# Kernel optimization log

Hardware: AMD Instinct MI355X
Metric: run time of the kernel (lower is better)

Reference implementation:

```python
import jax, jax.numpy as jnp
import numpy as np
from jax import lax

L, B, H, Z, V = 64, 32, 256, 256, 32000  # steps, max_ast_depth, hidden=units, latent, vocab


def setup_inputs() -> dict:
    key = jax.random.key(0)
    ks = jax.random.split(key, 32)
    p = lambda i, shape: jax.random.normal(ks[i], shape, dtype=jnp.float32) * 0.05
    inp = {
        "nodes": jax.random.randint(ks[0], (L, B), 0, V),
        "edges": jax.random.randint(ks[1], (L, B), 0, 2) > 0,
        "enc_init": jax.random.normal(ks[2], (B, H), dtype=jnp.float32) * 0.001,
        "eps": jax.random.normal(ks[3], (B, Z), dtype=jnp.float32),
        "emb": p(4, (V, H)),
    }
    for j, n in enumerate(["enc_c", "enc_s", "dec_c", "dec_s"]):
        inp[n + "_Wih"] = p(5 + 4 * j, (3 * H, H))
        inp[n + "_Whh"] = p(6 + 4 * j, (3 * H, H))
        inp[n + "_bih"] = p(7 + 4 * j, (3 * H,))
        inp[n + "_bhh"] = p(8 + 4 * j, (3 * H,))
    inp["W_mean"] = p(21, (Z, H)); inp["b_mean"] = p(22, (Z,))
    inp["W_logv"] = p(23, (Z, H)); inp["b_logv"] = p(24, (Z,))
    inp["W_l2h"] = p(25, (H, Z)); inp["b_l2h"] = p(26, (H,))
    inp["W_voc"] = p(27, (V, H)); inp["b_voc"] = p(28, (V,))
    return inp


def _gru_cell(Wih, Whh, bih, bhh, x, h):
    # torch.nn.GRU single-layer cell; x, h: [B, H]
    gi = x @ Wih.T + bih
    gh = h @ Whh.T + bhh
    ir, iz, inn = jnp.split(gi, 3, axis=-1)
    hr, hz, hn = jnp.split(gh, 3, axis=-1)
    r = jax.nn.sigmoid(ir + hr)
    zg = jax.nn.sigmoid(iz + hz)
    n = jnp.tanh(inn + r * hn)
    return (1.0 - zg) * n + zg * h


def _tree_rnn(pc, ps, emb_nodes, edges, h0):
    # emb_nodes: [L, B, H], edges: [L, B] bool, h0: [B, H]
    # each step runs child & sibling GRUs on the SAME state, selects per node by edge
    def step(h, xe):
        x, e = xe
        hc = _gru_cell(*pc, x, h)
        hs = _gru_cell(*ps, x, h)
        h_new = jnp.where(e[:, None], hc, hs)
        return h_new, h_new  # 1-layer GRU, seq_len 1: output == new state
    h_final, outs = lax.scan(step, h0, (emb_nodes, edges))
    return outs, h_final  # outs: [L, B, H]


def reference(nodes, edges, enc_init, eps, emb,
              enc_c_Wih, enc_c_Whh, enc_c_bih, enc_c_bhh,
              enc_s_Wih, enc_s_Whh, enc_s_bih, enc_s_bhh,
              dec_c_Wih, dec_c_Whh, dec_c_bih, dec_c_bhh,
              dec_s_Wih, dec_s_Whh, dec_s_bih, dec_s_bhh,
              W_mean, b_mean, W_logv, b_logv, W_l2h, b_l2h, W_voc, b_voc):
    x = emb[nodes]  # [L, B, H]
    _, h_enc = _tree_rnn((enc_c_Wih, enc_c_Whh, enc_c_bih, enc_c_bhh),
                         (enc_s_Wih, enc_s_Whh, enc_s_bih, enc_s_bhh),
                         x, edges, enc_init)
    mean = h_enc @ W_mean.T + b_mean          # [B, Z]
    logv = h_enc @ W_logv.T + b_logv
    z = eps * jnp.exp(0.5 * logv) + mean      # reparameterization
    h0 = z @ W_l2h.T + b_l2h                  # decoder initial state [B, H]
    outs, _ = _tree_rnn((dec_c_Wih, dec_c_Whh, dec_c_bih, dec_c_bhh),
                        (dec_s_Wih, dec_s_Whh, dec_s_bih, dec_s_bhh),
                        x, edges, h0)         # [L, B, H]
    logits = outs @ W_voc.T + b_voc           # [L, B, V]
    logp = jax.nn.log_softmax(logits, axis=-1)
    return logp, mean, logv, z
```

## Files before the change

### kernel.cpp

```cpp
#include <hip/hip_runtime.h>
#include <stdint.h>

typedef unsigned short u16;
typedef unsigned int u32;

#define L_STEPS 64
#define B_SZ 32
#define H_SZ 256
#define Z_SZ 256
#define V_SZ 32000
#define H2 128
#define G3H 768

typedef _Float16 h2_t __attribute__((ext_vector_type(2)));
typedef _Float16 f16x8 __attribute__((ext_vector_type(8)));
typedef float f32x4 __attribute__((ext_vector_type(4)));

#define WHH2_OFF   0
#define WIH2_OFF   393216
#define WM2_OFF    786432
#define WLV2_OFF   819200
#define WL2H2_OFF  851968
#define GI2_OFF    884736
#define OUTS2_OFF  4030464
#define W16_OFF    4292608
#define WS_NEEDED  ((size_t)(W16_OFF + 4096000) * 4)

#define NPART 250

#define OUT_MEAN_OFF  65536000
#define OUT_LOGV_OFF  65544192
#define OUT_Z_OFF     65552384

__device__ __forceinline__ float fdot2(h2_t a, h2_t b, float c){
#if __has_builtin(__builtin_amdgcn_fdot2)
  return __builtin_amdgcn_fdot2(a, b, c, false);
#else
  return c + (float)a.x*(float)b.x + (float)a.y*(float)b.y;
#endif
}
__device__ __forceinline__ float sigm(float x){ return 1.f/(1.f + __expf(-x)); }

struct PackTArgs { const float2* src[11]; int n_h2[11]; int dstoff[11]; };

__global__ __launch_bounds__(256) void k_packt(PackTArgs p, h2_t* wsh){
  int m = blockIdx.y;
  int r = blockIdx.x*256 + threadIdx.x;
  if (r >= p.n_h2[m]) return;
  int row = r >> 7, k2 = r & 127;
  float2 f = p.src[m][r];
  h2_t h; h.x = (_Float16)f.x; h.y = (_Float16)f.y;
  int off = (((row>>6)*32 + (k2>>2))*64 + (row&63))*4 + (k2&3);
  wsh[p.dstoff[m] + off] = h;
}

__global__ __launch_bounds__(256) void k_packv(const float2* __restrict__ src,
                                               h2_t* __restrict__ dst, int total){
  int idx = blockIdx.x*256 + threadIdx.x;
  if (idx >= total) return;
  float2 f = src[idx];
  h2_t h; h.x = (_Float16)f.x; h.y = (_Float16)f.y;
  dst[idx] = h;
}

struct GiArgs { const float* bih[4]; };

__global__ __launch_bounds__(256) void k_gi(const int* __restrict__ nodes,
                                            const float* __restrict__ emb,
                                            const h2_t* __restrict__ wih2,
                                            GiArgs ga, h2_t* __restrict__ gi2){
  int l = blockIdx.x, g = blockIdx.y, t = threadIdx.x;
  __shared__ __align__(16) h2_t x2[B_SZ*132];
  #pragma unroll
  for (int it=0; it<16; ++it){
    int lin = it*256 + t;
    int bb = lin >> 7, k2 = lin & 127;
    int node = nodes[l*B_SZ + bb];
    float2 f = ((const float2*)(emb + (size_t)node*H_SZ))[k2];
    h2_t r; r.x=(_Float16)f.x; r.y=(_Float16)f.y;
    x2[bb*132 + k2] = r;
  }
  __syncthreads();
  const float* bih = ga.bih[g];
  for (int jc=0; jc<3; ++jc){
    int j = jc*256 + t;
    float acc[32];
    #pragma unroll
    for (int bb=0;bb<32;bb++) acc[bb]=0.f;
    const float4* Wv = (const float4*)wih2 + (size_t)g*24576 + (j>>6)*2048 + (j&63);
    #pragma unroll 2
    for (int kb=0;kb<32;kb++){
      union{float4 f; h2_t h[4];} w4;
      w4.f = Wv[kb*64];
      #pragma unroll
      for (int kc=0;kc<4;kc++){
        h2_t w = w4.h[kc];
        int k2 = kb*4 + kc;
        #pragma unroll
        for (int bb=0;bb<32;bb++) acc[bb] = fdot2(x2[bb*132+k2], w, acc[bb]);
      }
    }
    float bvv = bih[j];
    int base = (g*2048 + l*B_SZ)*384 + (j>>1);
    #pragma unroll
    for (int bb=0;bb<32;bb++){
      float own = acc[bb] + bvv;
      float oth = __shfl_xor(own, 1, 64);
      if (!(t&1)){
        h2_t r; r.x=(_Float16)own; r.y=(_Float16)oth;
        gi2[base + bb*384] = r;
      }
    }
  }
}

struct ScanArgs {
  const float* bhh[4];
  const float* b_mean; const float* b_logv; const float* b_l2h;
  const float* enc_init; const float* eps;
};

__global__ __launch_bounds__(768) void k_scan(const int* __restrict__ edges, ScanArgs sa,
                                              const h2_t* __restrict__ wsh,
                                              h2_t* __restrict__ outs2,
                                              float* __restrict__ out){
  int b = blockIdx.x, t = threadIdx.x;
  int i = t & 255, gate = t >> 8;
  int lane = t & 63, rb = t >> 6;
  __shared__ float h_lds[H_SZ];
  __shared__ __align__(16) h2_t hs2[H2];
  __shared__ float g_lds[512];
  __shared__ float s_bhh[4*G3H];
  __shared__ int s_edge[L_STEPS];
  const _Float16* gi_all = (const _Float16*)(wsh + GI2_OFF);

  if (t < H_SZ) h_lds[t] = sa.enc_init[b*H_SZ + t];
  if (t < L_STEPS) s_edge[t] = edges[t*B_SZ + b];
  #pragma unroll
  for (int m=0;m<4;m++) s_bhh[m*G3H + t] = sa.bhh[m][t];
  __syncthreads();
  if (t < H2){ h2_t r; r.x=(_Float16)h_lds[2*t]; r.y=(_Float16)h_lds[2*t+1]; hs2[t]=r; }
  __syncthreads();

  const float4* hsv = (const float4*)hs2;

  for (int ph=0; ph<2; ++ph){
    for (int l=0; l<L_STEPS; ++l){
      int e = s_edge[l];
      int gsel = (ph ? 2 : 0) + (e ? 0 : 1);
      float gi0=0.f, gi1=0.f, gi2v=0.f;
      if (t < H_SZ){
        const _Float16* gr = gi_all + (size_t)(gsel*2048 + l*B_SZ + b)*G3H;
        gi0  = (float)gr[i];
        gi1  = (float)gr[256+i];
        gi2v = (float)gr[512+i];
      }
      float bv = s_bhh[gsel*G3H + t];
      const float4* Wv = (const float4*)wsh + (size_t)gsel*24576 + rb*2048 + lane;
      float a0=0.f,a1=0.f,a2=0.f,a3=0.f;
      #pragma unroll 8
      for (int kb=0;kb<32;kb++){
        union{float4 f; h2_t h[4];} w, x;
        w.f = Wv[kb*64];
        x.f = hsv[kb];
        a0 = fdot2(x.h[0], w.h[0], a0);
        a1 = fdot2(x.h[1], w.h[1], a1);
        a2 = fdot2(x.h[2], w.h[2], a2);
        a3 = fdot2(x.h[3], w.h[3], a3);
      }
      float acc = (a0+a1)+(a2+a3) + bv;
      if (gate) g_lds[(gate-1)*256 + i] = acc;
      __syncthreads();
      if (t < H_SZ){
        float r = sigm(gi0 + acc);
        float z = sigm(gi1 + g_lds[i]);
        float n = tanhf(gi2v + r*g_lds[256+i]);
        float hn = (1.f - z)*n + z*h_lds[i];
        h_lds[i] = hn;
        float ho = __shfl_xor(hn, 1, 64);
        if (!(i & 1)){
          h2_t pk; pk.x=(_Float16)hn; pk.y=(_Float16)ho;
          hs2[i>>1] = pk;
          if (ph) outs2[(l*B_SZ + b)*H2 + (i>>1)] = pk;
        }
      }
      __syncthreads();
    }

    if (ph == 0){
      if (t < H_SZ){
        const float4* WmV = (const float4*)(wsh + WM2_OFF)  + (t>>6)*2048 + (t&63);
        const float4* WlV = (const float4*)(wsh + WLV2_OFF) + (t>>6)*2048 + (t&63);
        float m0=0.f,m1=0.f,m2=0.f,m3=0.f, l0=0.f,l1=0.f,l2=0.f,l3=0.f;
        #pragma unroll 8
        for (int kb=0;kb<32;kb++){
          union{float4 f; h2_t h[4];} wm, wl, x;
          x.f  = hsv[kb];
          wm.f = WmV[kb*64];
          wl.f = WlV[kb*64];
          m0=fdot2(x.h[0],wm.h[0],m0); m1=fdot2(x.h[1],wm.h[1],m1);
          m2=fdot2(x.h[2],wm.h[2],m2); m3=fdot2(x.h[3],wm.h[3],m3);
          l0=fdot2(x.h[0],wl.h[0],l0); l1=fdot2(x.h[1],wl.h[1],l1);
          l2=fdot2(x.h[2],wl.h[2],l2); l3=fdot2(x.h[3],wl.h[3],l3);
        }
        float am = (m0+m1)+(m2+m3) + sa.b_mean[t];
        float al = (l0+l1)+(l2+l3) + sa.b_logv[t];
        float zv = sa.eps[b*Z_SZ + t] * __expf(0.5f*al) + am;
        out[OUT_MEAN_OFF + b*Z_SZ + t] = am;
        out[OUT_LOGV_OFF + b*Z_SZ + t] = al;
        out[OUT_Z_OFF    + b*Z_SZ + t] = zv;
        h_lds[t] = zv;
      }
      __syncthreads();
      if (t < H2){ h2_t r; r.x=(_Float16)h_lds[2*t]; r.y=(_Float16)h_lds[2*t+1]; hs2[t]=r; }
      __syncthreads();
      float h0v = 0.f;
      if (t < H_SZ){
        const float4* WzV = (const float4*)(wsh + WL2H2_OFF) + (t>>6)*2048 + (t&63);
        float z0=0.f,z1=0.f,z2=0.f,z3=0.f;
        #pragma unroll 8
        for (int kb=0;kb<32;kb++){
          union{float4 f; h2_t h[4];} w, x;
          x.f = hsv[kb];
          w.f = WzV[kb*64];
          z0=fdot2(x.h[0],w.h[0],z0); z1=fdot2(x.h[1],w.h[1],z1);
          z2=fdot2(x.h[2],w.h[2],z2); z3=fdot2(x.h[3],w.h[3],z3);
        }
        h0v = (z0+z1)+(z2+z3) + sa.b_l2h[t];
      }
      __syncthreads();
      if (t < H_SZ) h_lds[t] = h0v;
      __syncthreads();
      if (t < H2){ h2_t r; r.x=(_Float16)h_lds[2*t]; r.y=(_Float16)h_lds[2*t+1]; hs2[t]=r; }
      __syncthreads();
    }
  }
}

__global__ __launch_bounds__(256) void k_gemmS(const h2_t* __restrict__ outs2,
                                               const _Float16* __restrict__ wv16,
                                               const float* __restrict__ bvoc,
                                               float* __restrict__ outf,
                                               float* __restrict__ part){
  int t = threadIdx.x;
  int lane = t & 63, w = t >> 6;
  int wm = w & 1, wn = w >> 1;
  int Mb = blockIdx.x * 64, Nb = blockIdx.y * 128;
  int lr = lane & 15, lq = lane >> 4;

  __shared__ __align__(16) _Float16 As[64*64];
  __shared__ __align__(16) _Float16 Bs[128*64];
  __shared__ float red[2][64][2];

  f32x4 acc[2][4];
  #pragma unroll
  for (int mi=0;mi<2;mi++)
    #pragma unroll
    for (int nj=0;nj<4;nj++) acc[mi][nj] = (f32x4){0.f,0.f,0.f,0.f};

  for (int kc=0; kc<4; ++kc){
    #pragma unroll
    for (int q=0;q<2;q++){
      int ch = q*256 + t;
      int row = ch >> 3, kb = ch & 7;
      float4 d = ((const float4*)(outs2 + (size_t)(Mb + row)*H2 + kc*32))[kb];
      ((float4*)As)[row*8 + (kb ^ (row & 7))] = d;
    }
    #pragma unroll
    for (int q=0;q<4;q++){
      int ch = q*256 + t;
      int row = ch >> 3, kb = ch & 7;
      float4 d = ((const float4*)(wv16 + (size_t)(Nb + row)*H_SZ + kc*64))[kb];
      ((float4*)Bs)[row*8 + (kb ^ (row & 7))] = d;
    }
    __syncthreads();
    union{float4 f; f16x8 h;} af[2][2], bf[4][2];
    #pragma unroll
    for (int mi=0;mi<2;mi++)
      #pragma unroll
      for (int kk=0;kk<2;kk++){
        int row = wm*32 + mi*16 + lr;
        int ks = kk*4 + lq;
        af[mi][kk].f = ((const float4*)As)[row*8 + (ks ^ (row & 7))];
      }
    #pragma unroll
    for (int nj=0;nj<4;nj++)
      #pragma unroll
      for (int kk=0;kk<2;kk++){
        int row = wn*64 + nj*16 + lr;
        int ks = kk*4 + lq;
        bf[nj][kk].f = ((const float4*)Bs)[row*8 + (ks ^ (row & 7))];
      }
    #pragma unroll
    for (int kk=0;kk<2;kk++)
      #pragma unroll
      for (int mi=0;mi<2;mi++)
        #pragma unroll
        for (int nj=0;nj<4;nj++)
          acc[mi][nj] = __builtin_amdgcn_mfma_f32_16x16x32_f16(
                          af[mi][kk].h, bf[nj][kk].h, acc[mi][nj], 0, 0, 0);
    __syncthreads();
  }

  float bias[4];
  #pragma unroll
  for (int nj=0;nj<4;nj++) bias[nj] = bvoc[Nb + wn*64 + nj*16 + lr];
  #pragma unroll
  for (int mi=0;mi<2;mi++){
    int r0 = Mb + wm*32 + mi*16 + lq*4;
    #pragma unroll
    for (int rg=0;rg<4;rg++){
      float v[4];
      #pragma unroll
      for (int nj=0;nj<4;nj++){
        v[nj] = acc[mi][nj][rg] + bias[nj];
        outf[(size_t)(r0 + rg)*V_SZ + (Nb + wn*64 + nj*16 + lr)] = v[nj];
      }
      float mx = fmaxf(fmaxf(v[0],v[1]), fmaxf(v[2],v[3]));
      #pragma unroll
      for (int o=1;o<16;o<<=1) mx = fmaxf(mx, __shfl_xor(mx, o, 64));
      float sv = __expf(v[0]-mx)+__expf(v[1]-mx)+__expf(v[2]-mx)+__expf(v[3]-mx);
      #pragma unroll
      for (int o=1;o<16;o<<=1) sv += __shfl_xor(sv, o, 64);
      if (lr == 0){
        int rloc = wm*32 + mi*16 + lq*4 + rg;
        red[wn][rloc][0] = mx;
        red[wn][rloc][1] = sv;
      }
    }
  }
  __syncthreads();
  if (t < 64){
    float m0 = red[0][t][0], s0 = red[0][t][1];
    float m1 = red[1][t][0], s1 = red[1][t][1];
    float M = fmaxf(m0, m1);
    float S = s0*__expf(m0-M) + s1*__expf(m1-M);
    int row = Mb + t;
    part[((size_t)row*NPART + blockIdx.y)*2 + 0] = M;
    part[((size_t)row*NPART + blockIdx.y)*2 + 1] = S;
  }
}

__global__ __launch_bounds__(256) void k_lsered(const float* __restrict__ part,
                                                float* __restrict__ lse){
  int r = blockIdx.x*256 + threadIdx.x;
  if (r >= 2048) return;
  const float* pr = part + (size_t)r*NPART*2;
  float M = -1e30f;
  for (int p=0;p<NPART;p++) M = fmaxf(M, pr[p*2]);
  float S = 0.f;
  for (int p=0;p<NPART;p++) S += pr[p*2+1] * __expf(pr[p*2] - M);
  lse[r] = M + logf(S);
}

__global__ __launch_bounds__(256) void k_final(float* __restrict__ outf,
                                               const float* __restrict__ lse){
  int r = blockIdx.x;
  float l = lse[r];
  float4* row = (float4*)(outf + (size_t)r * V_SZ);
  for (int c = threadIdx.x; c < 8000; c += 256){
    float4 v = row[c];
    v.x -= l; v.y -= l; v.z -= l; v.w -= l;
    row[c] = v;
  }
}

__global__ __launch_bounds__(512) void k_gemm(const h2_t* __restrict__ outs2,
                                              const float* __restrict__ wv,
                                              const float* __restrict__ bvoc,
                                              float* __restrict__ outf){
  int t = threadIdx.x;
  int vq = t & 31, rq = t >> 5;
  int Nb = blockIdx.x * 256, Mb = blockIdx.y * 128;
  __shared__ __align__(16) h2_t A[16*128];
  __shared__ __align__(16) h2_t Bss[16*256];
  float acc[8][8];
  #pragma unroll
  for (int a=0;a<8;a++){
    #pragma unroll
    for (int c=0;c<8;c++) acc[a][c]=0.f;
  }

  for (int kc=0;kc<8;kc++){
    {
      int r = t >> 2, q = t & 3;
      union{float4 f; h2_t h[4];} u;
      u.f = ((const float4*)(outs2 + (Mb + r)*H2 + kc*16))[q];
      #pragma unroll
      for (int uu=0; uu<4; ++uu) A[(q*4+uu)*128 + r] = u.h[uu];
    }
    {
      int v = t >> 1, q = t & 1;
      const float* wrow = wv + (size_t)(Nb + v)*H_SZ + kc*32 + q*16;
      #pragma unroll
      for (int p=0;p<4;p++){
        float4 f = ((const float4*)wrow)[p];
        h2_t h0; h0.x=(_Float16)f.x; h0.y=(_Float16)f.y;
        h2_t h1; h1.x=(_Float16)f.z; h1.y=(_Float16)f.w;
        Bss[(q*8+p*2  )*256 + v] = h0;
        Bss[(q*8+p*2+1)*256 + v] = h1;
      }
    }
    __syncthreads();
    #pragma unroll 2
    for (int k2=0;k2<16;k2++){
      union{float4 f; h2_t h[4];} a0, a1, b0, b1;
      a0.f = *(const float4*)(A  + k2*128 + rq*8);
      a1.f = *(const float4*)(A  + k2*128 + rq*8 + 4);
      b0.f = *(const float4*)(Bss + k2*256 + vq*4);
      b1.f = *(const float4*)(Bss + k2*256 + vq*4 + 128);
      #pragma unroll
      for (int ii=0;ii<8;ii++){
        h2_t av = (ii<4)? a0.h[ii] : a1.h[ii-4];
        #pragma unroll
        for (int jj=0;jj<8;jj++){
          h2_t bv = (jj<4)? b0.h[jj] : b1.h[jj-4];
          acc[ii][jj] = fdot2(av, bv, acc[ii][jj]);
        }
      }
    }
    __syncthreads();
  }

  float bias0[4], bias1[4];
  #pragma unroll
  for (int jj=0;jj<4;jj++){
    bias0[jj] = bvoc[Nb + 4*vq + jj];
    bias1[jj] = bvoc[Nb + 128 + 4*vq + jj];
  }
  #pragma unroll
  for (int ii=0;ii<8;ii++){
    size_t base = (size_t)(Mb + rq*8 + ii)*(size_t)V_SZ + (size_t)Nb;
    float4 o0, o1;
    o0.x = acc[ii][0]+bias0[0]; o0.y = acc[ii][1]+bias0[1];
    o0.z = acc[ii][2]+bias0[2]; o0.w = acc[ii][3]+bias0[3];
    o1.x = acc[ii][4]+bias1[0]; o1.y = acc[ii][5]+bias1[1];
    o1.z = acc[ii][6]+bias1[2]; o1.w = acc[ii][7]+bias1[3];
    *(float4*)(outf + base + 4*vq)       = o0;
    *(float4*)(outf + base + 128 + 4*vq) = o1;
  }
}

__global__ __launch_bounds__(256) void k_softmax(float* __restrict__ outf){
  int rrow = blockIdx.x, t = threadIdx.x;
  float4* row = (float4*)(outf + (size_t)rrow * V_SZ);
  float4 v[32];
  #pragma unroll
  for (int i=0;i<31;i++) v[i] = row[i*256 + t];
  if (t < 64) v[31] = row[7936 + t];
  else { v[31].x = -1e30f; v[31].y = -1e30f; v[31].z = -1e30f; v[31].w = -1e30f; }

  float m = -1e30f;
  #pragma unroll
  for (int i=0;i<32;i++) m = fmaxf(m, fmaxf(fmaxf(v[i].x, v[i].y), fmaxf(v[i].z, v[i].w)));

  __shared__ float sred[4];
  __shared__ float sbc;
  int wid = t >> 6, lane = t & 63;
  #pragma unroll
  for (int o=32;o;o>>=1) m = fmaxf(m, __shfl_xor(m, o, 64));
  if (lane==0) sred[wid] = m;
  __syncthreads();
  if (t==0) sbc = fmaxf(fmaxf(sred[0],sred[1]), fmaxf(sred[2],sred[3]));
  __syncthreads();
  m = sbc;
  __syncthreads();

  float s = 0.f;
  #pragma unroll
  for (int i=0;i<32;i++){
    s += __expf(v[i].x - m) + __expf(v[i].y - m) + __expf(v[i].z - m) + __expf(v[i].w - m);
  }
  #pragma unroll
  for (int o=32;o;o>>=1) s += __shfl_xor(s, o, 64);
  if (lane==0) sred[wid] = s;
  __syncthreads();
  if (t==0) sbc = sred[0]+sred[1]+sred[2]+sred[3];
  __syncthreads();
  float lse = m + logf(sbc);

  #pragma unroll
  for (int i=0;i<31;i++){
    v[i].x -= lse; v[i].y -= lse; v[i].z -= lse; v[i].w -= lse;
    row[i*256 + t] = v[i];
  }
  if (t < 64){
    v[31].x -= lse; v[31].y -= lse; v[31].z -= lse; v[31].w -= lse;
    row[7936 + t] = v[31];
  }
}

extern "C" void kernel_launch(void* const* d_in, const int* in_sizes, int n_in,
                              void* d_out, int out_size, void* d_ws, size_t ws_size,
                              hipStream_t stream){
  const int* nodes = (const int*)d_in[0];
  const int* edges = (const int*)d_in[1];
  h2_t* wsh = (h2_t*)d_ws;
  float* outf = (float*)d_out;
  bool mfma_path = (ws_size >= WS_NEEDED);

  PackTArgs pt;
  const int srcidx[11] = {6,10,14,18, 5,9,13,17, 21,23,25};
  for (int k=0;k<11;k++){
    pt.src[k] = (const float2*)d_in[srcidx[k]];
    pt.n_h2[k] = (k < 8) ? 98304 : 32768;
  }
  for (int k=0;k<4;k++) pt.dstoff[k]   = WHH2_OFF + k*98304;
  for (int k=0;k<4;k++) pt.dstoff[4+k] = WIH2_OFF + k*98304;
  pt.dstoff[8] = WM2_OFF; pt.dstoff[9] = WLV2_OFF; pt.dstoff[10] = WL2H2_OFF;
  k_packt<<<dim3(384,11), dim3(256), 0, stream>>>(pt, wsh);

  if (mfma_path)
    k_packv<<<dim3(16000), dim3(256), 0, stream>>>((const float2*)d_in[27],
                                                   wsh + W16_OFF, 4096000);

  GiArgs ga;
  ga.bih[0]=(const float*)d_in[7];  ga.bih[1]=(const float*)d_in[11];
  ga.bih[2]=(const float*)d_in[15]; ga.bih[3]=(const float*)d_in[19];
  k_gi<<<dim3(64,4), dim3(256), 0, stream>>>(nodes, (const float*)d_in[4], wsh + WIH2_OFF, ga, wsh + GI2_OFF);

  ScanArgs sa;
  sa.bhh[0]=(const float*)d_in[8];  sa.bhh[1]=(const float*)d_in[12];
  sa.bhh[2]=(const float*)d_in[16]; sa.bhh[3]=(const float*)d_in[20];
  sa.b_mean=(const float*)d_in[22]; sa.b_logv=(const float*)d_in[24]; sa.b_l2h=(const float*)d_in[26];
  sa.enc_init=(const float*)d_in[2]; sa.eps=(const float*)d_in[3];
  k_scan<<<dim3(32), dim3(768), 0, stream>>>(edges, sa, wsh, wsh + OUTS2_OFF, outf);

  if (mfma_path){
    float* part = (float*)(wsh + GI2_OFF);
    float* lse  = part + 2048*NPART*2;
    k_gemmS<<<dim3(32,250), dim3(256), 0, stream>>>(wsh + OUTS2_OFF,
                                                    (const _Float16*)(wsh + W16_OFF),
                                                    (const float*)d_in[28], outf, part);
    k_lsered<<<dim3(8), dim3(256), 0, stream>>>(part, lse);
    k_final<<<dim3(2048), dim3(256), 0, stream>>>(outf, lse);
  } else {
    k_gemm<<<dim3(125,16), dim3(512), 0, stream>>>(wsh + OUTS2_OFF, (const float*)d_in[27],
                                                   (const float*)d_in[28], outf);
    k_softmax<<<dim3(2048), dim3(256), 0, stream>>>(outf);
  }
}
```

Measured before the change: 1.053 ms.

## Stage GEMM logits through LDS for coalesced stores; fuse LSE reduce into final pass

```diff
diff --git a/kernel.cpp b/kernel.cpp
--- a/kernel.cpp
+++ b/kernel.cpp
@@ -248,9 +248,11 @@
   int Mb = blockIdx.x * 64, Nb = blockIdx.y * 128;
   int lr = lane & 15, lq = lane >> 4;
 
-  __shared__ __align__(16) _Float16 As[64*64];
-  __shared__ __align__(16) _Float16 Bs[128*64];
-  __shared__ float red[2][64][2];
+  __shared__ __align__(16) char smem_raw[25600];
+  _Float16* As   = (_Float16*)smem_raw;
+  _Float16* Bs   = (_Float16*)(smem_raw + 8192);
+  float*    Ctile= (float*)smem_raw;
+  float*    red  = (float*)(smem_raw + 24576);
 
   f32x4 acc[2][4];
   #pragma unroll
@@ -306,62 +308,113 @@
   #pragma unroll
   for (int nj=0;nj<4;nj++) bias[nj] = bvoc[Nb + wn*64 + nj*16 + lr];
   #pragma unroll
-  for (int mi=0;mi<2;mi++){
-    int r0 = Mb + wm*32 + mi*16 + lq*4;
+  for (int mi=0;mi<2;mi++)
+    #pragma unroll
+    for (int nj=0;nj<4;nj++)
+      #pragma unroll
+      for (int rg=0;rg<4;rg++) acc[mi][nj][rg] += bias[nj];
+
+  #pragma unroll
+  for (int mi=0;mi<2;mi++)
     #pragma unroll
     for (int rg=0;rg<4;rg++){
-      float v[4];
-      #pragma unroll
-      for (int nj=0;nj<4;nj++){
-        v[nj] = acc[mi][nj][rg] + bias[nj];
-        outf[(size_t)(r0 + rg)*V_SZ + (Nb + wn*64 + nj*16 + lr)] = v[nj];
-      }
-      float mx = fmaxf(fmaxf(v[0],v[1]), fmaxf(v[2],v[3]));
+      float mx = fmaxf(fmaxf(acc[mi][0][rg],acc[mi][1][rg]),
+                       fmaxf(acc[mi][2][rg],acc[mi][3][rg]));
       #pragma unroll
       for (int o=1;o<16;o<<=1) mx = fmaxf(mx, __shfl_xor(mx, o, 64));
-      float sv = __expf(v[0]-mx)+__expf(v[1]-mx)+__expf(v[2]-mx)+__expf(v[3]-mx);
+      float sv = __expf(acc[mi][0][rg]-mx)+__expf(acc[mi][1][rg]-mx)
+               + __expf(acc[mi][2][rg]-mx)+__expf(acc[mi][3][rg]-mx);
       #pragma unroll
       for (int o=1;o<16;o<<=1) sv += __shfl_xor(sv, o, 64);
       if (lr == 0){
         int rloc = wm*32 + mi*16 + lq*4 + rg;
-        red[wn][rloc][0] = mx;
-        red[wn][rloc][1] = sv;
-      }
-    }
-  }
-  __syncthreads();
-  if (t < 64){
-    float m0 = red[0][t][0], s0 = red[0][t][1];
-    float m1 = red[1][t][0], s1 = red[1][t][1];
-    float M = fmaxf(m0, m1);
-    float S = s0*__expf(m0-M) + s1*__expf(m1-M);
-    int row = Mb + t;
-    part[((size_t)row*NPART + blockIdx.y)*2 + 0] = M;
-    part[((size_t)row*NPART + blockIdx.y)*2 + 1] = S;
-  }
-}
-
-__global__ __launch_bounds__(256) void k_lsered(const float* __restrict__ part,
-                                                float* __restrict__ lse){
-  int r = blockIdx.x*256 + threadIdx.x;
-  if (r >= 2048) return;
+        red[(wn*64 + rloc)*2 + 0] = mx;
+        red[(wn*64 + rloc)*2 + 1] = sv;
+      }
+    }
+
+  #pragma unroll
+  for (int h=0; h<2; ++h){
+    if (wn == h){
+      #pragma unroll
+      for (int mi=0;mi<2;mi++)
+        #pragma unroll
+        for (int nj=0;nj<4;nj++)
+          #pragma unroll
+          for (int rg=0;rg<4;rg++)
+            Ctile[(wm*32 + mi*16 + lq*4 + rg)*68 + nj*16 + lr] = acc[mi][nj][rg];
+    }
+    __syncthreads();
+    #pragma unroll
+    for (int i=0;i<4;i++){
+      int f4 = i*256 + t;
+      int row = f4 >> 4, c4 = f4 & 15;
+      float4 v = *(const float4*)&Ctile[row*68 + c4*4];
+      *(float4*)(outf + (size_t)(Mb + row)*V_SZ + Nb + h*64 + c4*4) = v;
+    }
+    if (h == 0 && t < 64){
+      float m0 = red[t*2], s0 = red[t*2+1];
+      float m1 = red[(64+t)*2], s1 = red[(64+t)*2+1];
+      float M = fmaxf(m0, m1);
+      float S = s0*__expf(m0-M) + s1*__expf(m1-M);
+      part[((size_t)(Mb + t)*NPART + blockIdx.y)*2 + 0] = M;
+      part[((size_t)(Mb + t)*NPART + blockIdx.y)*2 + 1] = S;
+    }
+    __syncthreads();
+  }
+}
+
+__global__ __launch_bounds__(512) void k_finalred(float* __restrict__ outf,
+                                                  const float* __restrict__ part){
+  int r = blockIdx.x, t = threadIdx.x;
+  int wid = t >> 6, lane = t & 63;
+  __shared__ float sm[8], ss[8], sbc[2];
+
   const float* pr = part + (size_t)r*NPART*2;
-  float M = -1e30f;
-  for (int p=0;p<NPART;p++) M = fmaxf(M, pr[p*2]);
-  float S = 0.f;
-  for (int p=0;p<NPART;p++) S += pr[p*2+1] * __expf(pr[p*2] - M);
-  lse[r] = M + logf(S);
-}
-
-__global__ __launch_bounds__(256) void k_final(float* __restrict__ outf,
-                                               const float* __restrict__ lse){
-  int r = blockIdx.x;
-  float l = lse[r];
+  float m = -1e30f, s = 0.f;
+  if (t < NPART){ m = pr[t*2]; s = pr[t*2+1]; }
+  float M = m;
+  #pragma unroll
+  for (int o=32;o;o>>=1) M = fmaxf(M, __shfl_xor(M, o, 64));
+  if (lane==0) sm[wid] = M;
+  __syncthreads();
+  if (t==0){
+    float x = sm[0];
+    #pragma unroll
+    for (int q=1;q<8;q++) x = fmaxf(x, sm[q]);
+    sbc[0] = x;
+  }
+  __syncthreads();
+  M = sbc[0];
+  float sv = (t < NPART) ? s*__expf(m - M) : 0.f;
+  #pragma unroll
+  for (int o=32;o;o>>=1) sv += __shfl_xor(sv, o, 64);
+  if (lane==0) ss[wid] = sv;
+  __syncthreads();
+  if (t==0){
+    float S = 0.f;
+    #pragma unroll
+    for (int q=0;q<8;q++) S += ss[q];
+    sbc[1] = M + logf(S);
+  }
+  __syncthreads();
+  float lse = sbc[1];
+
   float4* row = (float4*)(outf + (size_t)r * V_SZ);
-  for (int c = threadIdx.x; c < 8000; c += 256){
+  #pragma unroll 5
+  for (int i=0;i<15;i++){
+    int c = i*512 + t;
     float4 v = row[c];
-    v.x -= l; v.y -= l; v.z -= l; v.w -= l;
+    v.x -= lse; v.y -= lse; v.z -= lse; v.w -= lse;
     row[c] = v;
+  }
+  {
+    int c = 15*512 + t;
+    if (c < 8000){
+      float4 v = row[c];
+      v.x -= lse; v.y -= lse; v.z -= lse; v.w -= lse;
+      row[c] = v;
+    }
   }
 }
 
@@ -528,12 +581,10 @@
 
   if (mfma_path){
     float* part = (float*)(wsh + GI2_OFF);
-    float* lse  = part + 2048*NPART*2;
     k_gemmS<<<dim3(32,250), dim3(256), 0, stream>>>(wsh + OUTS2_OFF,
                                                     (const _Float16*)(wsh + W16_OFF),
                                                     (const float*)d_in[28], outf, part);
-    k_lsered<<<dim3(8), dim3(256), 0, stream>>>(part, lse);
-    k_final<<<dim3(2048), dim3(256), 0, stream>>>(outf, lse);
+    k_finalred<<<dim3(2048), dim3(512), 0, stream>>>(outf, part);
   } else {
     k_gemm<<<dim3(125,16), dim3(512), 0, stream>>>(wsh + OUTS2_OFF, (const float*)d_in[27],
                                                    (const float*)d_in[28], outf);
```

Measured after the change: 991.9 us. -5.8%, faster.
